# Performance work log

Measured on AMD Instinct MI355X. Metric: run time of the kernel, lower is better.

Reference implementation:

```python
import jax, jax.numpy as jnp
import numpy as np

N_ROWS, N_COLS = 4, 4
EPS = 1e-5


def setup_inputs() -> dict:
    key = jax.random.key(0)
    ks = jax.random.split(key, 4)
    x = jax.random.normal(ks[0], (32, 32, 256, 256), dtype=jnp.float32)
    gamma = jnp.ones((32,), dtype=jnp.float32)
    beta = jnp.zeros((32,), dtype=jnp.float32)
    prelu_a = jnp.full((1,), 0.25, dtype=jnp.float32)  # torch PReLU default init
    conv_w = jax.random.normal(ks[1], (32, 32, 3, 3), dtype=jnp.float32) * (1.0 / np.sqrt(32 * 9))
    conv_b = jax.random.normal(ks[2], (32,), dtype=jnp.float32) * 0.01
    return {"x": x, "gamma": gamma, "beta": beta, "prelu_a": prelu_a,
            "conv_w": conv_w, "conv_b": conv_b}


def reference(x, gamma, beta, prelu_a, conv_w, conv_b):
    B, C, H, W = x.shape
    rh, rw = H // N_ROWS, W // N_COLS
    # Fold the region grid into a leading region axis: [R, B, C, rh, rw]
    xr = x.reshape(B, C, N_ROWS, rh, N_COLS, rw)
    xr = xr.transpose(2, 4, 0, 1, 3, 5).reshape(N_ROWS * N_COLS, B, C, rh, rw)
    # BatchNorm (training mode): per-region, per-channel stats over (B, rh, rw)
    mean = xr.mean(axis=(1, 3, 4), keepdims=True)
    var = jnp.mean((xr - mean) ** 2, axis=(1, 3, 4), keepdims=True)  # biased var
    g = gamma[None, None, :, None, None]
    b = beta[None, None, :, None, None]
    y = (xr - mean) * jax.lax.rsqrt(var + EPS) * g + b
    # PReLU with a single shared slope
    y = jnp.where(y > 0, y, prelu_a[0] * y)
    # Conv2d 3x3 pad=1 applied per region (zero padding at region borders)
    yb = y.reshape(N_ROWS * N_COLS * B, C, rh, rw)
    out = jax.lax.conv_general_dilated(
        yb, conv_w, window_strides=(1, 1), padding=((1, 1), (1, 1)),
        dimension_numbers=("NCHW", "OIHW", "NCHW"))
    out = out + conv_b[None, :, None, None]
    # Reassemble region grid -> full image
    out = out.reshape(N_ROWS, N_COLS, B, C, rh, rw)
    out = out.transpose(2, 3, 0, 4, 1, 5).reshape(B, C, H, W)
    return out
```

## Files before the change

### kernel.cpp

```cpp
#include <hip/hip_runtime.h>
#include <hip/hip_bf16.h>


#define EPS 1e-5f

typedef float f32x4 __attribute__((ext_vector_type(4)));
typedef __bf16 bf16x8 __attribute__((ext_vector_type(8)));
typedef short short8 __attribute__((ext_vector_type(8)));

__device__ inline short f2bf(float f) {
  union { __hip_bfloat16 h; short s; } u;
  u.h = __float2bfloat16(f);
  return u.s;
}

__global__ __launch_bounds__(256) void stats_partial(
    const float* __restrict__ x, float* __restrict__ ws_sum,
    float* __restrict__ ws_sq) {
  int plane = blockIdx.x;
  const float* base = x + (size_t)plane * 65536;
  int t = threadIdx.x;
  float s[4] = {0.f, 0.f, 0.f, 0.f}, q[4] = {0.f, 0.f, 0.f, 0.f};
#pragma unroll
  for (int R = 0; R < 4; ++R) {
#pragma unroll
    for (int ii = 0; ii < 16; ++ii) {
      int idx4 = (R * 16 + ii) * 256 + t;
      float4 v = *reinterpret_cast<const float4*>(base + (size_t)idx4 * 4);
      s[R] += (v.x + v.y) + (v.z + v.w);
      q[R] += (v.x * v.x + v.y * v.y) + (v.z * v.z + v.w * v.w);
    }
  }
#pragma unroll
  for (int R = 0; R < 4; ++R) {
#pragma unroll
    for (int off = 8; off; off >>= 1) {
      s[R] += __shfl_down(s[R], off);
      q[R] += __shfl_down(q[R], off);
    }
  }
  __shared__ float red[2][4][4][4];
  int lane = t & 63, wv = t >> 6;
  if ((lane & 15) == 0) {
    int Cc = lane >> 4;
#pragma unroll
    for (int R = 0; R < 4; ++R) {
      red[0][wv][Cc][R] = s[R];
      red[1][wv][Cc][R] = q[R];
    }
  }
  __syncthreads();
  if (t < 16) {
    int R = t >> 2, Cc = t & 3;
    float S = 0.f, Q = 0.f;
#pragma unroll
    for (int w = 0; w < 4; ++w) {
      S += red[0][w][Cc][R];
      Q += red[1][w][Cc][R];
    }
    ws_sum[plane * 16 + t] = S;
    ws_sq[plane * 16 + t] = Q;
  }
}

__global__ __launch_bounds__(256) void weights_prep(
    const float* __restrict__ conv_w, unsigned short* __restrict__ wfrag) {
  int idx = blockIdx.x * 256 + threadIdx.x;
  if (idx >= 18 * 64) return;
  int lane = idx & 63;
  int th = idx >> 6;
  int t = th >> 1, h = th & 1;
  int dy = t / 3, dx = t - dy * 3;
  int oc = h * 16 + (lane & 15);
  int ic0 = (lane >> 4) * 8;
#pragma unroll
  for (int j = 0; j < 8; ++j) {
    float w = conv_w[((oc * 32 + ic0 + j) * 3 + dy) * 3 + dx];
    wfrag[(size_t)idx * 8 + j] = (unsigned short)f2bf(w);
  }
}

__global__ __launch_bounds__(256) void conv_mfma(
    const float* __restrict__ x, const unsigned short* __restrict__ wfrag,
    const float* __restrict__ conv_b, const float* __restrict__ prelu_a,
    const float* __restrict__ ws_sum, const float* __restrict__ ws_sq,
    const float* __restrict__ gamma, const float* __restrict__ beta,
    float* __restrict__ out) {
  __shared__ short lds_y[10 * 64 * 32];

  int blk0 = blockIdx.x;
  int blk = (blk0 & 7) * 512 + (blk0 >> 3);
  int rt = blk & 7;
  int p = (blk >> 3) & 15;
  int b = blk >> 7;
  int R = p >> 2, Cc = p & 3;
  int h0 = rt * 8;
  int tid = threadIdx.x;
  int lane = tid & 63;
  float pa = prelu_a[0];

  float* abuf = (float*)lds_y;
  if (tid < 32) {
    int c = tid;
    float S = 0.f, Q = 0.f;
#pragma unroll
    for (int bb = 0; bb < 32; ++bb) {
      int idx = (bb * 32 + c) * 16 + p;
      S += ws_sum[idx];
      Q += ws_sq[idx];
    }
    const float inv = 1.0f / 131072.0f;
    float mean = S * inv;
    float var = Q * inv - mean * mean;
    float rstd = rsqrtf(var + EPS);
    float a = rstd * gamma[c];
    abuf[c] = a;
    abuf[32 + c] = beta[c] - mean * a;
  }
  __syncthreads();

  int s = (tid >> 4) & 3;
  int c4 = tid & 15;
  int srb = tid >> 6;
  int ic0 = s * 8;

  float a_r[8], b_r[8];
#pragma unroll
  for (int j = 0; j < 8; ++j) {
    a_r[j] = abuf[ic0 + j];
    b_r[j] = abuf[32 + ic0 + j];
  }
  __syncthreads();

  auto stage_load = [&](f32x4(&vv)[8], int sr) {
    int lr = h0 - 1 + sr;
#pragma unroll
    for (int kk = 0; kk < 8; ++kk) vv[kk] = f32x4{0.f, 0.f, 0.f, 0.f};
    if ((unsigned)lr < 64u) {
      const float* xp =
          x + (((size_t)(b * 32 + ic0) * 256 + R * 64 + lr) * 256) + Cc * 64 +
          c4 * 4;
#pragma unroll
      for (int kk = 0; kk < 8; ++kk)
        vv[kk] = *reinterpret_cast<const f32x4*>(xp + (size_t)kk * 65536);
    }
  };
  auto stage_write = [&](const f32x4(&vv)[8], int sr) {
#pragma unroll
    for (int j = 0; j < 4; ++j) {
      short8 pk;
#pragma unroll
      for (int kk = 0; kk < 8; ++kk) {
        float e = fmaf(a_r[kk], vv[kk][j], b_r[kk]);
        e = e > 0.f ? e : pa * e;
        pk[kk] = f2bf(e);
      }
      int col = c4 * 4 + j;
      int slot = (s + (col >> 1)) & 3;
      *reinterpret_cast<short8*>(&lds_y[(sr * 64 + col) * 32 + slot * 8]) = pk;
    }
  };

  {
    f32x4 va[8], vb[8], vc[8];
    stage_load(va, srb);
    stage_load(vb, srb + 4);
    stage_write(va, srb);
    if (tid < 128) stage_load(vc, srb + 8);
    stage_write(vb, srb + 4);
    if (tid < 128) stage_write(vc, srb + 8);
  }
  __syncthreads();

  bf16x8 wf[18];
#pragma unroll
  for (int th = 0; th < 18; ++th) {
    short8 sv =
        *reinterpret_cast<const short8*>(wfrag + ((size_t)th * 64 + lane) * 8);
    wf[th] = __builtin_bit_cast(bf16x8, sv);
  }
  int l15 = lane & 15, l4 = lane >> 4;
  f32x4 bias0, bias1;
#pragma unroll
  for (int i = 0; i < 4; ++i) {
    bias0[i] = conv_b[l4 * 4 + i];
    bias1[i] = conv_b[16 + l4 * 4 + i];
  }

  int wv = tid >> 6;
  const short8 z8 = {0, 0, 0, 0, 0, 0, 0, 0};
  for (int g = 0; g < 8; ++g) {
    int gi = wv * 8 + g;
    int r = gi >> 2;
    int c0 = (gi & 3) * 16;
    f32x4 acc0 = bias0, acc1 = bias1;
#pragma unroll
    for (int t9 = 0; t9 < 9; ++t9) {
      const int dy = t9 / 3, dx = t9 - dy * 3;
      int sr = r + dy;
      int col_in = c0 + l15 + dx - 1;
      int colc = col_in & 63;
      int slot = (l4 + (colc >> 1)) & 3;
      short8 sv = *reinterpret_cast<const short8*>(
          &lds_y[(sr * 64 + colc) * 32 + slot * 8]);
      if (dx == 0) {
        if (c0 == 0 && l15 == 0) sv = z8;
      }
      if (dx == 2) {
        if (c0 == 48 && l15 == 15) sv = z8;
      }
      bf16x8 bv = __builtin_bit_cast(bf16x8, sv);
      acc0 = __builtin_amdgcn_mfma_f32_16x16x32_bf16(wf[t9 * 2], bv, acc0, 0, 0, 0);
      acc1 = __builtin_amdgcn_mfma_f32_16x16x32_bf16(wf[t9 * 2 + 1], bv, acc1, 0, 0, 0);
    }
    int grow = R * 64 + h0 + r;
    int gcol = Cc * 64 + c0 + l15;
    float* ob = out + (size_t)b * 2097152 + (size_t)grow * 256 + gcol;
#pragma unroll
    for (int i = 0; i < 4; ++i) {
      __builtin_nontemporal_store(acc0[i], &ob[(size_t)(l4 * 4 + i) * 65536]);
      __builtin_nontemporal_store(acc1[i],
                                  &ob[(size_t)(16 + l4 * 4 + i) * 65536]);
    }
  }
}

extern "C" void kernel_launch(void* const* d_in, const int* in_sizes, int n_in,
                              void* d_out, int out_size, void* d_ws,
                              size_t ws_size, hipStream_t stream) {
  const float* x = (const float*)d_in[0];
  const float* gamma = (const float*)d_in[1];
  const float* beta = (const float*)d_in[2];
  const float* prelu_a = (const float*)d_in[3];
  const float* conv_w = (const float*)d_in[4];
  const float* conv_b = (const float*)d_in[5];
  float* out = (float*)d_out;

  float* ws = (float*)d_ws;
  float* ws_sum = ws;
  float* ws_sq = ws + 16384;
  unsigned short* wfrag = (unsigned short*)(ws + 32768);

  weights_prep<<<5, 256, 0, stream>>>(conv_w, wfrag);
  stats_partial<<<1024, 256, 0, stream>>>(x, ws_sum, ws_sq);
  conv_mfma<<<4096, 256, 0, stream>>>(x, wfrag, conv_b, prelu_a, ws_sum, ws_sq,
                                      gamma, beta, out);
}
```

Before: 172.5 us.

## Hoist BN finalize into separate kernel and halve conv row tile

The per-block reduction of batch statistics into BN scale/shift moves into a single stats_finalize kernel, so each conv block just loads precomputed per-region coefficients instead of re-reducing 32 partials and taking two barriers. The conv tile shrinks from 8 to 4 output rows per block, doubling the grid to 8192 blocks and cutting LDS to 6 staged rows. This aims to cut per-block prologue latency and improve occupancy. In exchange the halo overhead grows from 10/8 to 6/4 rows of input reloaded, and there is an extra kernel launch.

```diff
diff --git a/kernel.cpp b/kernel.cpp
--- a/kernel.cpp
+++ b/kernel.cpp
@@ -61,6 +61,28 @@
     ws_sum[plane * 16 + t] = S;
     ws_sq[plane * 16 + t] = Q;
   }
+}
+
+__global__ __launch_bounds__(512) void stats_finalize(
+    const float* __restrict__ ws_sum, const float* __restrict__ ws_sq,
+    const float* __restrict__ gamma, const float* __restrict__ beta,
+    float* __restrict__ wsA, float* __restrict__ wsB) {
+  int j = threadIdx.x;
+  int p = j >> 5, c = j & 31;
+  float S = 0.f, Q = 0.f;
+#pragma unroll
+  for (int b = 0; b < 32; ++b) {
+    int idx = (b * 32 + c) * 16 + p;
+    S += ws_sum[idx];
+    Q += ws_sq[idx];
+  }
+  const float inv = 1.0f / 131072.0f;
+  float mean = S * inv;
+  float var = Q * inv - mean * mean;
+  float rstd = rsqrtf(var + EPS);
+  float a = rstd * gamma[c];
+  wsA[p * 32 + c] = a;
+  wsB[p * 32 + c] = beta[c] - mean * a;
 }
 
 __global__ __launch_bounds__(256) void weights_prep(
@@ -83,54 +105,32 @@
 __global__ __launch_bounds__(256) void conv_mfma(
     const float* __restrict__ x, const unsigned short* __restrict__ wfrag,
     const float* __restrict__ conv_b, const float* __restrict__ prelu_a,
-    const float* __restrict__ ws_sum, const float* __restrict__ ws_sq,
-    const float* __restrict__ gamma, const float* __restrict__ beta,
+    const float* __restrict__ wsA, const float* __restrict__ wsB,
     float* __restrict__ out) {
-  __shared__ short lds_y[10 * 64 * 32];
+  __shared__ short lds_y[6 * 64 * 32];
 
   int blk0 = blockIdx.x;
-  int blk = (blk0 & 7) * 512 + (blk0 >> 3);
-  int rt = blk & 7;
-  int p = (blk >> 3) & 15;
-  int b = blk >> 7;
+  int blk = (blk0 & 7) * 1024 + (blk0 >> 3);
+  int rt = blk & 15;
+  int p = (blk >> 4) & 15;
+  int b = blk >> 8;
   int R = p >> 2, Cc = p & 3;
-  int h0 = rt * 8;
+  int h0 = rt * 4;
   int tid = threadIdx.x;
   int lane = tid & 63;
   float pa = prelu_a[0];
-
-  float* abuf = (float*)lds_y;
-  if (tid < 32) {
-    int c = tid;
-    float S = 0.f, Q = 0.f;
-#pragma unroll
-    for (int bb = 0; bb < 32; ++bb) {
-      int idx = (bb * 32 + c) * 16 + p;
-      S += ws_sum[idx];
-      Q += ws_sq[idx];
-    }
-    const float inv = 1.0f / 131072.0f;
-    float mean = S * inv;
-    float var = Q * inv - mean * mean;
-    float rstd = rsqrtf(var + EPS);
-    float a = rstd * gamma[c];
-    abuf[c] = a;
-    abuf[32 + c] = beta[c] - mean * a;
-  }
-  __syncthreads();
 
   int s = (tid >> 4) & 3;
   int c4 = tid & 15;
   int srb = tid >> 6;
   int ic0 = s * 8;
 
-  float a_r[8], b_r[8];
-#pragma unroll
-  for (int j = 0; j < 8; ++j) {
-    a_r[j] = abuf[ic0 + j];
-    b_r[j] = abuf[32 + ic0 + j];
-  }
-  __syncthreads();
+  float4 a0 = *reinterpret_cast<const float4*>(wsA + p * 32 + ic0);
+  float4 a1 = *reinterpret_cast<const float4*>(wsA + p * 32 + ic0 + 4);
+  float4 bb0 = *reinterpret_cast<const float4*>(wsB + p * 32 + ic0);
+  float4 bb1 = *reinterpret_cast<const float4*>(wsB + p * 32 + ic0 + 4);
+  float a_r[8] = {a0.x, a0.y, a0.z, a0.w, a1.x, a1.y, a1.z, a1.w};
+  float b_r[8] = {bb0.x, bb0.y, bb0.z, bb0.w, bb1.x, bb1.y, bb1.z, bb1.w};
 
   auto stage_load = [&](f32x4(&vv)[8], int sr) {
     int lr = h0 - 1 + sr;
@@ -162,13 +162,11 @@
   };
 
   {
-    f32x4 va[8], vb[8], vc[8];
+    f32x4 va[8], vb[8];
     stage_load(va, srb);
-    stage_load(vb, srb + 4);
+    if (tid < 128) stage_load(vb, 4 + srb);
     stage_write(va, srb);
-    if (tid < 128) stage_load(vc, srb + 8);
-    stage_write(vb, srb + 4);
-    if (tid < 128) stage_write(vc, srb + 8);
+    if (tid < 128) stage_write(vb, 4 + srb);
   }
   __syncthreads();
 
@@ -189,10 +187,9 @@
 
   int wv = tid >> 6;
   const short8 z8 = {0, 0, 0, 0, 0, 0, 0, 0};
-  for (int g = 0; g < 8; ++g) {
-    int gi = wv * 8 + g;
-    int r = gi >> 2;
-    int c0 = (gi & 3) * 16;
+  for (int g = 0; g < 4; ++g) {
+    int r = wv;
+    int c0 = g * 16;
     f32x4 acc0 = bias0, acc1 = bias1;
 #pragma unroll
     for (int t9 = 0; t9 < 9; ++t9) {
@@ -239,10 +236,13 @@
   float* ws = (float*)d_ws;
   float* ws_sum = ws;
   float* ws_sq = ws + 16384;
-  unsigned short* wfrag = (unsigned short*)(ws + 32768);
+  float* wsA = ws + 32768;
+  float* wsB = ws + 33280;
+  unsigned short* wfrag = (unsigned short*)(ws + 33792);
 
   weights_prep<<<5, 256, 0, stream>>>(conv_w, wfrag);
   stats_partial<<<1024, 256, 0, stream>>>(x, ws_sum, ws_sq);
-  conv_mfma<<<4096, 256, 0, stream>>>(x, wfrag, conv_b, prelu_a, ws_sum, ws_sq,
-                                      gamma, beta, out);
-}
+  stats_finalize<<<1, 512, 0, stream>>>(ws_sum, ws_sq, gamma, beta, wsA, wsB);
+  conv_mfma<<<8192, 256, 0, stream>>>(x, wfrag, conv_b, prelu_a, wsA, wsB,
+                                      out);
+}
```

New measurement: 177.0 us. 2.6% more time.
